# Kernel optimization log

Hardware: AMD Instinct MI355X
Metric: run time of the kernel (lower is better)

## Reference

```python
import jax, jax.numpy as jnp
import numpy as np

B, T, D = 4, 2048, 1024
H = 4                      # fla GatedLinearAttention default num_heads
K = D; V = D               # expand_k = expand_v = 1
DK = K // H; DV = V // H   # 256 each
LOW = 16                   # gate_low_rank_dim default
GLN = 16.0                 # gate_logit_normalizer default


def _layernorm(x, w, b, eps=1e-5):
    mu = x.mean(-1, keepdims=True)
    xc = x - mu
    var = (xc * xc).mean(-1, keepdims=True)
    return xc * jax.lax.rsqrt(var + eps) * w + b


def _rmsnorm(x, w, eps=1e-5):
    ms = (x * x).mean(-1, keepdims=True)
    return x * jax.lax.rsqrt(ms + eps) * w


def _gla_scan(q, k, v, gk):
    # q,k,gk: [B,T,H,DK]; v: [B,T,H,DV]
    scale = DK ** -0.5
    qT = jnp.moveaxis(q * scale, 1, 0)  # [T,B,H,DK]
    kT = jnp.moveaxis(k, 1, 0)
    vT = jnp.moveaxis(v, 1, 0)
    gT = jnp.moveaxis(gk, 1, 0)

    def step(h, inp):
        qt, kt, vt, gt = inp  # [B,H,DK]/[B,H,DV]
        h = h * jnp.exp(gt)[..., None] + kt[..., :, None] * vt[..., None, :]
        o = jnp.einsum('bhk,bhkv->bhv', qt, h)
        return h, o

    h0 = jnp.zeros((q.shape[0], H, DK, DV), q.dtype)
    _, oT = jax.lax.scan(step, h0, (qT, kT, vT, gT))
    return jnp.moveaxis(oT, 0, 1)  # [B,T,H,DV]


def setup_inputs() -> dict:
    key = jax.random.key(0)
    ks = jax.random.split(key, 12)
    rn = lambda k, s: jax.random.normal(k, s, jnp.float32) * 0.02
    return {
        'x': jax.random.normal(ks[0], (B, T, D), jnp.float32),
        'ln1_w': jnp.ones((D,), jnp.float32), 'ln1_b': jnp.zeros((D,), jnp.float32),
        'Wq': rn(ks[1], (D, K)), 'Wk': rn(ks[2], (D, K)), 'Wv': rn(ks[3], (D, V)),
        'Wg': rn(ks[4], (D, V)),
        'Wgk1': rn(ks[5], (D, LOW)), 'Wgk2': rn(ks[6], (LOW, K)), 'bgk2': jnp.zeros((K,), jnp.float32),
        'rms_w': jnp.ones((DV,), jnp.float32),
        'Wo': rn(ks[7], (V, D)),
        'ln2_w': jnp.ones((D,), jnp.float32), 'ln2_b': jnp.zeros((D,), jnp.float32),
        'W1': rn(ks[8], (D, 3 * D)), 'b1': jnp.zeros((3 * D,), jnp.float32),
        'W2': rn(ks[9], (3 * D, D)), 'b2': jnp.zeros((D,), jnp.float32),
    }


def reference(x, ln1_w, ln1_b, Wq, Wk, Wv, Wg, Wgk1, Wgk2, bgk2, rms_w, Wo,
              ln2_w, ln2_b, W1, b1, W2, b2):
    b, t = x.shape[0], x.shape[1]
    xn = _layernorm(x, ln1_w, ln1_b)
    q = (xn @ Wq).reshape(b, t, H, DK)
    k = (xn @ Wk).reshape(b, t, H, DK)
    v = (xn @ Wv).reshape(b, t, H, DV)
    # low-rank forget gate: logsigmoid / gate_logit_normalizer
    gk = (jax.nn.log_sigmoid((xn @ Wgk1) @ Wgk2 + bgk2) / GLN).reshape(b, t, H, DK)
    o = _gla_scan(q, k, v, gk)                      # [B,T,H,DV]
    g = (xn @ Wg).reshape(b, t, H, DV)              # output gate
    o = _rmsnorm(o, rms_w) * (g * jax.nn.sigmoid(g))  # gated RMSNorm (swish gate)
    o = o.reshape(b, t, V) @ Wo
    x = x + o
    xn2 = _layernorm(x, ln2_w, ln2_b)
    h = jax.nn.leaky_relu(xn2 @ W1 + b1, 0.01)
    h = h * h                                        # LeakyReLU^2
    x = x + (h @ W2 + b2)
    return x
```

## Files before the change

### kernel.cpp

```cpp
#include <hip/hip_runtime.h>
#include <math.h>

#define BB 4
#define TT 2048
#define DD 1024
#define HH 4
#define DK 256
#define DV 256
#define RR 8192
#define CHK 64
#define NCHK 32
#define SS ((size_t)RR * DD)

typedef __bf16 bf16x8 __attribute__((ext_vector_type(8)));
typedef float f32x4 __attribute__((ext_vector_type(4)));

static __device__ inline unsigned short f2bf(float f) {
  unsigned int u = __float_as_uint(f);
  unsigned int r = (u + 0x7fffu + ((u >> 16) & 1u)) >> 16;
  return (unsigned short)r;
}
static __device__ inline float bf2f(unsigned short h) {
  return __uint_as_float(((unsigned int)h) << 16);
}

static __device__ __forceinline__ void gload16(const unsigned short* g,
                                               unsigned short* l) {
  __builtin_amdgcn_global_load_lds(
      (const __attribute__((address_space(1))) void*)g,
      (__attribute__((address_space(3))) void*)l, 16, 0, 0);
}

__global__ __launch_bounds__(256) void ln_kernel(const float* __restrict__ x,
                                                 const float* __restrict__ w,
                                                 const float* __restrict__ b,
                                                 unsigned short* __restrict__ yb) {
  int row = blockIdx.x;
  const float* xr = x + (size_t)row * DD;
  unsigned short* ybr = yb + (size_t)row * DD;
  int tid = threadIdx.x;

  float4 v = ((const float4*)xr)[tid];
  float s = v.x + v.y + v.z + v.w;
  float ss = v.x * v.x + v.y * v.y + v.z * v.z + v.w * v.w;
#pragma unroll
  for (int o = 32; o > 0; o >>= 1) {
    s += __shfl_down(s, o);
    ss += __shfl_down(ss, o);
  }
  __shared__ float ls[4], lss[4];
  int wid = tid >> 6;
  if ((tid & 63) == 0) { ls[wid] = s; lss[wid] = ss; }
  __syncthreads();
  float sum = ls[0] + ls[1] + ls[2] + ls[3];
  float sumsq = lss[0] + lss[1] + lss[2] + lss[3];
  float mu = sum * (1.0f / DD);
  float var = sumsq * (1.0f / DD) - mu * mu;
  float rs = rsqrtf(var + 1e-5f);

  float4 wv = ((const float4*)w)[tid];
  float4 bv = ((const float4*)b)[tid];
  ushort4 ob;
  ob.x = f2bf((v.x - mu) * rs * wv.x + bv.x);
  ob.y = f2bf((v.y - mu) * rs * wv.y + bv.y);
  ob.z = f2bf((v.z - mu) * rs * wv.z + bv.z);
  ob.w = f2bf((v.w - mu) * rs * wv.w + bv.w);
  ((ushort4*)ybr)[tid] = ob;
}

__global__ __launch_bounds__(256) void transpose_cast(const float* __restrict__ W,
                                                      unsigned short* __restrict__ Wt,
                                                      int K, int N) {
  __shared__ float t[32][33];
  int k0 = blockIdx.y * 32, n0 = blockIdx.x * 32;
  int tid = threadIdx.x;
  int tx = tid & 31, ty = tid >> 5;
#pragma unroll
  for (int i = 0; i < 4; ++i)
    t[ty + i * 8][tx] = W[(size_t)(k0 + ty + i * 8) * N + n0 + tx];
  __syncthreads();
#pragma unroll
  for (int i = 0; i < 4; ++i)
    Wt[(size_t)(n0 + ty + i * 8) * K + k0 + tx] = f2bf(t[tx][ty + i * 8]);
}

template <int EPI, int OUTBF>
__global__ __launch_bounds__(256) void gemm_bf16(
    const unsigned short* __restrict__ A,
    const unsigned short* __restrict__ Bt,
    const float* __restrict__ bias, const float* __restrict__ Res,
    void* __restrict__ Cv, int M, int N, int K) {
  __shared__ unsigned short As[2][128 * 64];
  __shared__ unsigned short Bs[2][128 * 64];
  int tid = threadIdx.x;
  int nwg = gridDim.x * gridDim.y;
  int wg = blockIdx.y * gridDim.x + blockIdx.x;
  int cpx = nwg >> 3;
  wg = (wg & 7) * cpx + (wg >> 3);
  int m0 = (wg / gridDim.x) * 128, n0 = (wg % gridDim.x) * 128;
  int lane = tid & 63;
  int w64 = tid & 192;
  int wid = tid >> 6;
  int wm = (wid >> 1) * 64, wn = (wid & 1) * 64;
  int fr = lane & 15, fq = lane >> 4;

  f32x4 acc[4][4] = {};

  auto STAGE = [&](int buf, int k0) {
#pragma unroll
    for (int j = 0; j < 4; ++j) {
      int gl = j * 256 + tid;
      int row = gl >> 3;
      int gs = (gl & 7) ^ (row & 7);
      gload16(&A[(size_t)(m0 + row) * K + k0 + gs * 8],
              &As[buf][(size_t)(j * 256 + w64) * 8]);
      gload16(&Bt[(size_t)(n0 + row) * K + k0 + gs * 8],
              &Bs[buf][(size_t)(j * 256 + w64) * 8]);
    }
  };

  STAGE(0, 0);
  asm volatile("s_waitcnt vmcnt(0)");
  __syncthreads();

  int cur = 0;
  for (int k0 = 0; k0 < K; k0 += 64) {
    if (k0 + 64 < K) STAGE(cur ^ 1, k0 + 64);

#pragma unroll
    for (int ph = 0; ph < 2; ++ph) {
      bf16x8 af[4], bv[4];
#pragma unroll
      for (int i = 0; i < 4; ++i) {
        int ra = wm + i * 16 + fr;
        af[i] = *(const bf16x8*)&As[cur][ra * 64 + (((ph * 4 + fq) ^ (ra & 7)) * 8)];
        int rb = wn + i * 16 + fr;
        bv[i] = *(const bf16x8*)&Bs[cur][rb * 64 + (((ph * 4 + fq) ^ (rb & 7)) * 8)];
      }
#pragma unroll
      for (int i = 0; i < 4; ++i)
#pragma unroll
        for (int jj = 0; jj < 4; ++jj)
          acc[i][jj] = __builtin_amdgcn_mfma_f32_16x16x32_bf16(af[i], bv[jj],
                                                               acc[i][jj], 0, 0, 0);
    }
    __syncthreads();
    cur ^= 1;
  }

  int col = lane & 15;
  int rbase = (lane >> 4) * 4;
#pragma unroll
  for (int i = 0; i < 4; ++i) {
#pragma unroll
    for (int j = 0; j < 4; ++j) {
      int n = n0 + wn + j * 16 + col;
      float bvv = (EPI == 2 || EPI == 4) ? bias[n] : 0.0f;
#pragma unroll
      for (int r = 0; r < 4; ++r) {
        int m = m0 + wm + i * 16 + rbase + r;
        float vv = acc[i][j][r] + bvv;
        if (EPI == 2) {
          float t = vv > 0.0f ? vv : 0.01f * vv;
          vv = t * t;
        }
        if (EPI == 3 || EPI == 4) vv += Res[(size_t)m * N + n];
        if (EPI == 5) {
          ((unsigned short*)Cv)[(size_t)(n >> 10) * SS + (size_t)m * 1024 +
                                (n & 1023)] = f2bf(vv);
        } else if (OUTBF) {
          ((unsigned short*)Cv)[(size_t)m * N + n] = f2bf(vv);
        } else {
          ((float*)Cv)[(size_t)m * N + n] = vv;
        }
      }
    }
  }
}

__global__ __launch_bounds__(256) void gk_kernel(const unsigned short* __restrict__ xn,
                                                 const float* __restrict__ Wgk1,
                                                 const float* __restrict__ Wgk2,
                                                 const float* __restrict__ bgk2,
                                                 unsigned short* __restrict__ gk) {
  int row = blockIdx.x;
  const unsigned short* xr = xn + (size_t)row * DD;
  int tid = threadIdx.x;

  float t16[16];
#pragma unroll
  for (int j = 0; j < 16; ++j) t16[j] = 0.0f;

#pragma unroll
  for (int dd = 0; dd < 4; ++dd) {
    int d = tid + dd * 256;
    float xv = bf2f(xr[d]);
    const float4* wrow = (const float4*)(Wgk1 + (size_t)d * 16);
#pragma unroll
    for (int q = 0; q < 4; ++q) {
      float4 wq = wrow[q];
      t16[q * 4 + 0] += xv * wq.x;
      t16[q * 4 + 1] += xv * wq.y;
      t16[q * 4 + 2] += xv * wq.z;
      t16[q * 4 + 3] += xv * wq.w;
    }
  }
#pragma unroll
  for (int j = 0; j < 16; ++j) {
    float s = t16[j];
#pragma unroll
    for (int o = 32; o > 0; o >>= 1) s += __shfl_down(s, o);
    t16[j] = s;
  }
  __shared__ float tmp[4][16];
  __shared__ float tf[16];
  int wid = tid >> 6;
  if ((tid & 63) == 0) {
#pragma unroll
    for (int j = 0; j < 16; ++j) tmp[wid][j] = t16[j];
  }
  __syncthreads();
  if (tid < 16) tf[tid] = tmp[0][tid] + tmp[1][tid] + tmp[2][tid] + tmp[3][tid];
  __syncthreads();

  float tl[16];
#pragma unroll
  for (int j = 0; j < 16; ++j) tl[j] = tf[j];

#pragma unroll
  for (int jj = 0; jj < 4; ++jj) {
    int n = tid * 4 + jj;
    float z = bgk2[n];
#pragma unroll
    for (int j = 0; j < 16; ++j) z += tl[j] * Wgk2[j * 1024 + n];
    float ls = fminf(z, 0.0f) - log1pf(expf(-fabsf(z)));
    gk[(size_t)row * 1024 + n] = f2bf(ls * (1.0f / 16.0f));
  }
}

__global__ __launch_bounds__(256) void gate_chunk(const unsigned short* __restrict__ gk,
                                                  unsigned short* __restrict__ q,
                                                  unsigned short* __restrict__ k,
                                                  float* __restrict__ ebC) {
  int bid = blockIdx.x;
  int c = bid & 31;
  int h = (bid >> 5) & 3;
  int b = bid >> 7;
  int tid = threadIdx.x;
  size_t base = ((size_t)b * TT + c * CHK) * 1024 + h * 256 + tid;

  const float scale = 0.0625f;
  float cum = 0.0f;
  for (int t = 0; t < CHK; ++t) {
    size_t a = base + (size_t)t * 1024;
    cum += bf2f(gk[a]);
    q[a] = f2bf(bf2f(q[a]) * expf(cum) * scale);
    k[a] = f2bf(bf2f(k[a]) * expf(-cum));
  }
  ebC[((b * 4 + h) * NCHK + c) * 256 + tid] = expf(cum);
}

template <int WITHE>
__global__ __launch_bounds__(256) void trans_kernel(const unsigned short* __restrict__ in,
                                                    const float* __restrict__ ebC,
                                                    unsigned short* __restrict__ outT) {
  __shared__ unsigned short T[64][68];
  int bid = blockIdx.x;
  int dkt = bid & 3;
  int ct = (bid >> 2) & 31;
  int bh = bid >> 7;
  int b = bh >> 2, h = bh & 3;
  int tid = threadIdx.x;
  int r = tid >> 4;
  int c4 = (tid & 15) * 4;
  size_t srcbase = ((size_t)b * TT + ct * 64) * 1024 + h * 256 + dkt * 64;
#pragma unroll
  for (int i = 0; i < 4; ++i)
    *(ushort4*)&T[r + i * 16][c4] =
        *(const ushort4*)&in[srcbase + (size_t)(r + i * 16) * 1024 + c4];
  __syncthreads();
  size_t outbase = (size_t)bh * 524288 + (size_t)(dkt * 64) * 2048 + ct * 64;
  const float* ep = ebC + ((size_t)bh * 32 + ct) * 256 + dkt * 64;
#pragma unroll
  for (int i = 0; i < 4; ++i) {
    int dkl = r + i * 16;
    float e = WITHE ? ep[dkl] : 1.0f;
    ushort4 o;
    o.x = f2bf(bf2f(T[c4 + 0][dkl]) * e);
    o.y = f2bf(bf2f(T[c4 + 1][dkl]) * e);
    o.z = f2bf(bf2f(T[c4 + 2][dkl]) * e);
    o.w = f2bf(bf2f(T[c4 + 3][dkl]) * e);
    *(ushort4*)&outT[outbase + (size_t)dkl * 2048 + c4] = o;
  }
}

__global__ __launch_bounds__(256) void u_gemm(const unsigned short* __restrict__ khatT,
                                              const unsigned short* __restrict__ vT,
                                              unsigned short* __restrict__ UT) {
  __shared__ unsigned short As[128 * 64];
  __shared__ unsigned short Bs[128 * 64];
  int tid = threadIdx.x;
  int bid = blockIdx.x;
  int tile = bid & 3;
  int bhc = bid >> 2;
  int bh = bhc >> 5, c = bhc & 31;
  int m0 = (tile >> 1) * 128, n0 = (tile & 1) * 128;
  const unsigned short* Ab = vT + (size_t)bh * 524288 + c * 64;
  const unsigned short* Bb = khatT + (size_t)bh * 524288 + c * 64;
  unsigned short* Cb = UT + (size_t)bhc * 65536;

  int lane = tid & 63;
  int w64 = tid & 192;
  int wid = tid >> 6;
  int wm = (wid >> 1) * 64, wn = (wid & 1) * 64;
  int fr = lane & 15, fq = lane >> 4;

  f32x4 acc[4][4] = {};

#pragma unroll
  for (int j = 0; j < 4; ++j) {
    int gl = j * 256 + tid;
    int row = gl >> 3;
    int gs = (gl & 7) ^ (row & 7);
    gload16(&Ab[(size_t)(m0 + row) * 2048 + gs * 8],
            &As[(size_t)(j * 256 + w64) * 8]);
    gload16(&Bb[(size_t)(n0 + row) * 2048 + gs * 8],
            &Bs[(size_t)(j * 256 + w64) * 8]);
  }
  __syncthreads();

#pragma unroll
  for (int ph = 0; ph < 2; ++ph) {
    bf16x8 af[4], bv[4];
#pragma unroll
    for (int i = 0; i < 4; ++i) {
      int ra = wm + i * 16 + fr;
      af[i] = *(const bf16x8*)&As[ra * 64 + (((ph * 4 + fq) ^ (ra & 7)) * 8)];
      int rb = wn + i * 16 + fr;
      bv[i] = *(const bf16x8*)&Bs[rb * 64 + (((ph * 4 + fq) ^ (rb & 7)) * 8)];
    }
#pragma unroll
    for (int i = 0; i < 4; ++i)
#pragma unroll
      for (int jj = 0; jj < 4; ++jj)
        acc[i][jj] = __builtin_amdgcn_mfma_f32_16x16x32_bf16(af[i], bv[jj],
                                                             acc[i][jj], 0, 0, 0);
  }

  int col = lane & 15;
  int rbase = (lane >> 4) * 4;
#pragma unroll
  for (int i = 0; i < 4; ++i)
#pragma unroll
    for (int j = 0; j < 4; ++j) {
      int n = n0 + wn + j * 16 + col;
#pragma unroll
      for (int r = 0; r < 4; ++r) {
        int m = m0 + wm + i * 16 + rbase + r;
        Cb[(size_t)m * 256 + n] = f2bf(acc[i][j][r]);
      }
    }
}

__global__ __launch_bounds__(256) void hscan(unsigned short* __restrict__ UH,
                                             const float* __restrict__ ebC) {
  int bid = blockIdx.x;
  int bh = bid >> 8, dv = bid & 255;
  int tid = threadIdx.x;
  size_t base = ((size_t)bh * NCHK) * 65536 + (size_t)dv * 256 + tid;
  const float* ebb = ebC + (size_t)bh * NCHK * 256;
  float h = 0.0f;
  for (int c = 0; c < NCHK; ++c) {
    size_t a = base + (size_t)c * 65536;
    float u = bf2f(UH[a]);
    UH[a] = f2bf(h);
    h = ebb[c * 256 + tid] * h + u;
  }
}

__global__ __launch_bounds__(256) void attn_fused(
    const unsigned short* __restrict__ qt, const unsigned short* __restrict__ kt,
    const unsigned short* __restrict__ vT, const unsigned short* __restrict__ HT,
    const unsigned short* __restrict__ gp, const float* __restrict__ rw,
    unsigned short* __restrict__ og) {
  __shared__ unsigned short Qs[64 * 264];
  __shared__ unsigned short KVH[256 * 72];
  __shared__ unsigned short Sb[64 * 64];
  __shared__ float red[64][4];

  int bid = blockIdx.x;
  int c = bid & 31;
  int bh = bid >> 5;
  int b = bh >> 2, h = bh & 3;
  size_t rowbase = ((size_t)b * TT + c * 64) * 1024 + h * 256;
  size_t vtbase = (size_t)bh * 524288 + c * 64;
  size_t htbase = ((size_t)(bh * 32 + c)) * 65536;
  int tid = threadIdx.x;
  int lane = tid & 63;
  int w = tid >> 6;
  int fr = lane & 15, fq = lane >> 4;

#pragma unroll
  for (int i = 0; i < 8; ++i) {
    int gg = tid + i * 256;
    int row = gg >> 5, gc = gg & 31;
    *(bf16x8*)&Qs[row * 264 + gc * 8] =
        *(const bf16x8*)&qt[rowbase + (size_t)row * 1024 + gc * 8];
    *(bf16x8*)&KVH[row * 264 + gc * 8] =
        *(const bf16x8*)&kt[rowbase + (size_t)row * 1024 + gc * 8];
  }
  __syncthreads();

  {
    f32x4 accs[4] = {};
#pragma unroll
    for (int ks = 0; ks < 8; ++ks) {
      bf16x8 af = *(const bf16x8*)&Qs[(w * 16 + fr) * 264 + ks * 32 + fq * 8];
#pragma unroll
      for (int si = 0; si < 4; ++si) {
        bf16x8 bf_ = *(const bf16x8*)&KVH[(si * 16 + fr) * 264 + ks * 32 + fq * 8];
        accs[si] = __builtin_amdgcn_mfma_f32_16x16x32_bf16(af, bf_, accs[si], 0, 0, 0);
      }
    }
#pragma unroll
    for (int si = 0; si < 4; ++si) {
#pragma unroll
      for (int r = 0; r < 4; ++r) {
        int t = w * 16 + fq * 4 + r;
        int s = si * 16 + fr;
        float val = (s <= t) ? accs[si][r] : 0.0f;
        Sb[t * 64 + (((s >> 3) ^ (t & 7)) * 8) + (s & 7)] = f2bf(val);
      }
    }
  }
  __syncthreads();

#pragma unroll
  for (int i = 0; i < 8; ++i) {
    int gg = tid + i * 256;
    int dv = gg >> 3, gc = gg & 7;
    *(bf16x8*)&KVH[dv * 72 + gc * 8] =
        *(const bf16x8*)&vT[vtbase + (size_t)dv * 2048 + gc * 8];
  }
  __syncthreads();

  int dv0 = w * 64;
  f32x4 acc[4][4] = {};

#pragma unroll
  for (int ks = 0; ks < 2; ++ks) {
    bf16x8 af[4], bv[4];
#pragma unroll
    for (int ti = 0; ti < 4; ++ti) {
      int t = ti * 16 + fr;
      af[ti] = *(const bf16x8*)&Sb[t * 64 + (((ks * 4 + fq) ^ (t & 7)) * 8)];
    }
#pragma unroll
    for (int nj = 0; nj < 4; ++nj)
      bv[nj] = *(const bf16x8*)&KVH[(dv0 + nj * 16 + fr) * 72 + ks * 32 + fq * 8];
#pragma unroll
    for (int ti = 0; ti < 4; ++ti)
#pragma unroll
      for (int nj = 0; nj < 4; ++nj)
        acc[ti][nj] = __builtin_amdgcn_mfma_f32_16x16x32_bf16(af[ti], bv[nj],
                                                              acc[ti][nj], 0, 0, 0);
  }

  for (int k4 = 0; k4 < 4; ++k4) {
    __syncthreads();
#pragma unroll
    for (int i = 0; i < 8; ++i) {
      int gg = tid + i * 256;
      int dv = gg >> 3, gc = gg & 7;
      *(bf16x8*)&KVH[dv * 72 + gc * 8] =
          *(const bf16x8*)&HT[htbase + (size_t)dv * 256 + k4 * 64 + gc * 8];
    }
    __syncthreads();
#pragma unroll
    for (int ks = 0; ks < 2; ++ks) {
      bf16x8 af[4], bv[4];
#pragma unroll
      for (int ti = 0; ti < 4; ++ti)
        af[ti] = *(const bf16x8*)&Qs[(ti * 16 + fr) * 264 + k4 * 64 + ks * 32 + fq * 8];
#pragma unroll
      for (int nj = 0; nj < 4; ++nj)
        bv[nj] = *(const bf16x8*)&KVH[(dv0 + nj * 16 + fr) * 72 + ks * 32 + fq * 8];
#pragma unroll
      for (int ti = 0; ti < 4; ++ti)
#pragma unroll
        for (int nj = 0; nj < 4; ++nj)
          acc[ti][nj] = __builtin_amdgcn_mfma_f32_16x16x32_bf16(af[ti], bv[nj],
                                                                acc[ti][nj], 0, 0, 0);
    }
  }

  float rstd[4][4];
#pragma unroll
  for (int ti = 0; ti < 4; ++ti) {
#pragma unroll
    for (int r = 0; r < 4; ++r) {
      float s = 0.0f;
#pragma unroll
      for (int nj = 0; nj < 4; ++nj) {
        float v = acc[ti][nj][r];
        s += v * v;
      }
      s += __shfl_xor(s, 1);
      s += __shfl_xor(s, 2);
      s += __shfl_xor(s, 4);
      s += __shfl_xor(s, 8);
      rstd[ti][r] = s;
    }
  }
  if (fr == 0) {
#pragma unroll
    for (int ti = 0; ti < 4; ++ti)
#pragma unroll
      for (int r = 0; r < 4; ++r)
        red[ti * 16 + fq * 4 + r][w] = rstd[ti][r];
  }
  __syncthreads();
#pragma unroll
  for (int ti = 0; ti < 4; ++ti) {
#pragma unroll
    for (int r = 0; r < 4; ++r) {
      int t = ti * 16 + fq * 4 + r;
      float tot = red[t][0] + red[t][1] + red[t][2] + red[t][3];
      rstd[ti][r] = rsqrtf(tot * (1.0f / 256.0f) + 1e-5f);
    }
  }
#pragma unroll
  for (int ti = 0; ti < 4; ++ti) {
#pragma unroll
    for (int nj = 0; nj < 4; ++nj) {
      int dv = dv0 + nj * 16 + fr;
      float rwv = rw[dv];
#pragma unroll
      for (int r = 0; r < 4; ++r) {
        int t = ti * 16 + fq * 4 + r;
        float gv = bf2f(gp[rowbase + (size_t)t * 1024 + dv]);
        float sw = gv / (1.0f + expf(-gv));
        og[rowbase + (size_t)t * 1024 + dv] =
            f2bf(acc[ti][nj][r] * rstd[ti][r] * rwv * sw);
      }
    }
  }
}

extern "C" void kernel_launch(void* const* d_in, const int* in_sizes, int n_in,
                              void* d_out, int out_size, void* d_ws,
                              size_t ws_size, hipStream_t stream) {
  const float* x = (const float*)d_in[0];
  const float* ln1_w = (const float*)d_in[1];
  const float* ln1_b = (const float*)d_in[2];
  const float* Wq = (const float*)d_in[3];
  const float* Wk = (const float*)d_in[4];
  const float* Wv = (const float*)d_in[5];
  const float* Wg = (const float*)d_in[6];
  const float* Wgk1 = (const float*)d_in[7];
  const float* Wgk2 = (const float*)d_in[8];
  const float* bgk2 = (const float*)d_in[9];
  const float* rms_w = (const float*)d_in[10];
  const float* Wo = (const float*)d_in[11];
  const float* ln2_w = (const float*)d_in[12];
  const float* ln2_b = (const float*)d_in[13];
  const float* W1 = (const float*)d_in[14];
  const float* b1 = (const float*)d_in[15];
  const float* W2 = (const float*)d_in[16];
  const float* b2 = (const float*)d_in[17];
  float* out = (float*)d_out;

  const size_t S = SS;
  unsigned short* actb = (unsigned short*)d_ws;
  unsigned short* qb = actb + S;
  unsigned short* kb = qb + S;
  unsigned short* vb = kb + S;
  unsigned short* gb = vb + S;
  unsigned short* gkb = gb + S;
  unsigned short* ogb = gkb + S;
  unsigned short* UH = ogb + 2 * S;
  float* ebC = (float*)(UH + 4 * S);
  unsigned short* Wqkvgt = (unsigned short*)(ebC + 131072);
  unsigned short* Wot = Wqkvgt + 4194304;
  unsigned short* W1t = Wot + 1048576;
  unsigned short* W2t = W1t + 3145728;
  unsigned short* khatT = gkb;
  unsigned short* vT = actb;
  float* x1 = (float*)kb;
  unsigned short* hb = UH;

  dim3 blk(256);

  transpose_cast<<<dim3(32, 32), blk, 0, stream>>>(Wq, Wqkvgt, 1024, 1024);
  transpose_cast<<<dim3(32, 32), blk, 0, stream>>>(Wk, Wqkvgt + 1048576, 1024, 1024);
  transpose_cast<<<dim3(32, 32), blk, 0, stream>>>(Wv, Wqkvgt + 2097152, 1024, 1024);
  transpose_cast<<<dim3(32, 32), blk, 0, stream>>>(Wg, Wqkvgt + 3145728, 1024, 1024);
  transpose_cast<<<dim3(32, 32), blk, 0, stream>>>(Wo, Wot, 1024, 1024);
  transpose_cast<<<dim3(96, 32), blk, 0, stream>>>(W1, W1t, 1024, 3072);
  transpose_cast<<<dim3(32, 96), blk, 0, stream>>>(W2, W2t, 3072, 1024);

  ln_kernel<<<RR, blk, 0, stream>>>(x, ln1_w, ln1_b, actb);

  dim3 g4096(4096 / 128, RR / 128);
  gemm_bf16<5, 1><<<g4096, blk, 0, stream>>>(actb, Wqkvgt, nullptr, nullptr, qb,
                                             RR, 4096, 1024);

  gk_kernel<<<RR, blk, 0, stream>>>(actb, Wgk1, Wgk2, bgk2, gkb);

  gate_chunk<<<BB * HH * NCHK, blk, 0, stream>>>(gkb, qb, kb, ebC);

  trans_kernel<1><<<16 * 32 * 4, blk, 0, stream>>>(kb, ebC, khatT);
  trans_kernel<0><<<16 * 32 * 4, blk, 0, stream>>>(vb, ebC, vT);

  u_gemm<<<16 * NCHK * 4, blk, 0, stream>>>(khatT, vT, UH);
  hscan<<<16 * 256, blk, 0, stream>>>(UH, ebC);

  attn_fused<<<16 * NCHK, blk, 0, stream>>>(qb, kb, vT, UH, gb, rms_w, ogb);

  dim3 g1024(1024 / 128, RR / 128);
  gemm_bf16<3, 0><<<g1024, blk, 0, stream>>>(ogb, Wot, nullptr, x, x1, RR, 1024, 1024);

  ln_kernel<<<RR, blk, 0, stream>>>(x1, ln2_w, ln2_b, actb);

  dim3 g3072(3072 / 128, RR / 128);
  gemm_bf16<2, 1><<<g3072, blk, 0, stream>>>(actb, W1t, b1, nullptr, hb, RR, 3072, 1024);

  gemm_bf16<4, 0><<<g1024, blk, 0, stream>>>(hb, W2t, b2, x1, out, RR, 1024, 3072);
}
```

Baseline: 445.2 us.

## Batch gk kernel over 16 rows, merge weight transposes, prefetch scan loads

The low-rank gate kernel now handles 16 rows per block. It stages the rows and a bf16 copy of Wgk1 in shared memory and keeps Wgk2 in registers, so the weights are reused across rows and there are fewer launches. Wgk1 is rounded to bf16, which slightly changes the gate numerics. The five square weight transposes become a single launch using a z-indexed grid. gate_chunk and hscan now load all their serial inputs into registers before running the recurrence, which shortens the memory-latency chain but uses more registers.

```diff
diff --git a/kernel.cpp b/kernel.cpp
--- a/kernel.cpp
+++ b/kernel.cpp
@@ -82,6 +82,27 @@
 #pragma unroll
   for (int i = 0; i < 4; ++i)
     Wt[(size_t)(n0 + ty + i * 8) * K + k0 + tx] = f2bf(t[tx][ty + i * 8]);
+}
+
+struct P5 {
+  const float* w[5];
+  unsigned short* o[5];
+};
+__global__ __launch_bounds__(256) void transpose5(P5 p) {
+  __shared__ float t[32][33];
+  int z = blockIdx.z;
+  const float* W = p.w[z];
+  unsigned short* Wt = p.o[z];
+  int k0 = blockIdx.y * 32, n0 = blockIdx.x * 32;
+  int tid = threadIdx.x;
+  int tx = tid & 31, ty = tid >> 5;
+#pragma unroll
+  for (int i = 0; i < 4; ++i)
+    t[ty + i * 8][tx] = W[(size_t)(k0 + ty + i * 8) * 1024 + n0 + tx];
+  __syncthreads();
+#pragma unroll
+  for (int i = 0; i < 4; ++i)
+    Wt[(size_t)(n0 + ty + i * 8) * 1024 + k0 + tx] = f2bf(t[tx][ty + i * 8]);
 }
 
 template <int EPI, int OUTBF>
@@ -183,58 +204,90 @@
                                                  const float* __restrict__ Wgk2,
                                                  const float* __restrict__ bgk2,
                                                  unsigned short* __restrict__ gk) {
-  int row = blockIdx.x;
-  const unsigned short* xr = xn + (size_t)row * DD;
-  int tid = threadIdx.x;
-
-  float t16[16];
-#pragma unroll
-  for (int j = 0; j < 16; ++j) t16[j] = 0.0f;
-
-#pragma unroll
-  for (int dd = 0; dd < 4; ++dd) {
-    int d = tid + dd * 256;
-    float xv = bf2f(xr[d]);
-    const float4* wrow = (const float4*)(Wgk1 + (size_t)d * 16);
-#pragma unroll
-    for (int q = 0; q < 4; ++q) {
-      float4 wq = wrow[q];
-      t16[q * 4 + 0] += xv * wq.x;
-      t16[q * 4 + 1] += xv * wq.y;
-      t16[q * 4 + 2] += xv * wq.z;
-      t16[q * 4 + 3] += xv * wq.w;
-    }
-  }
-#pragma unroll
-  for (int j = 0; j < 16; ++j) {
-    float s = t16[j];
-#pragma unroll
-    for (int o = 32; o > 0; o >>= 1) s += __shfl_down(s, o);
-    t16[j] = s;
-  }
-  __shared__ float tmp[4][16];
-  __shared__ float tf[16];
-  int wid = tid >> 6;
-  if ((tid & 63) == 0) {
-#pragma unroll
-    for (int j = 0; j < 16; ++j) tmp[wid][j] = t16[j];
-  }
-  __syncthreads();
-  if (tid < 16) tf[tid] = tmp[0][tid] + tmp[1][tid] + tmp[2][tid] + tmp[3][tid];
-  __syncthreads();
-
-  float tl[16];
-#pragma unroll
-  for (int j = 0; j < 16; ++j) tl[j] = tf[j];
-
-#pragma unroll
-  for (int jj = 0; jj < 4; ++jj) {
-    int n = tid * 4 + jj;
-    float z = bgk2[n];
-#pragma unroll
-    for (int j = 0; j < 16; ++j) z += tl[j] * Wgk2[j * 1024 + n];
-    float ls = fminf(z, 0.0f) - log1pf(expf(-fabsf(z)));
-    gk[(size_t)row * 1024 + n] = f2bf(ls * (1.0f / 16.0f));
+  __shared__ unsigned short Xs[16 * 1024];
+  __shared__ unsigned short W1s[1024 * 16];
+  __shared__ float Ts[16][16];
+  int r0 = blockIdx.x * 16;
+  int tid = threadIdx.x;
+
+#pragma unroll
+  for (int i = 0; i < 16; ++i) {
+    int idx = tid + i * 256;
+    ((ushort4*)Xs)[idx] = ((const ushort4*)(xn + (size_t)r0 * 1024))[idx];
+  }
+#pragma unroll
+  for (int i = 0; i < 16; ++i) {
+    int idx = tid + i * 256;
+    float4 w = ((const float4*)Wgk1)[idx];
+    ushort4 hh;
+    hh.x = f2bf(w.x); hh.y = f2bf(w.y); hh.z = f2bf(w.z); hh.w = f2bf(w.w);
+    ((ushort4*)W1s)[idx] = hh;
+  }
+  __syncthreads();
+
+  {
+    int r = tid >> 4, part = tid & 15;
+    float t16[16];
+#pragma unroll
+    for (int j = 0; j < 16; ++j) t16[j] = 0.0f;
+    for (int dd = 0; dd < 64; ++dd) {
+      int d = dd * 16 + part;
+      float xv = bf2f(Xs[r * 1024 + d]);
+      const ushort4* wr = (const ushort4*)&W1s[d * 16];
+#pragma unroll
+      for (int q4 = 0; q4 < 4; ++q4) {
+        ushort4 w = wr[q4];
+        t16[q4 * 4 + 0] += xv * bf2f(w.x);
+        t16[q4 * 4 + 1] += xv * bf2f(w.y);
+        t16[q4 * 4 + 2] += xv * bf2f(w.z);
+        t16[q4 * 4 + 3] += xv * bf2f(w.w);
+      }
+    }
+#pragma unroll
+    for (int j = 0; j < 16; ++j) {
+      float s = t16[j];
+      s += __shfl_xor(s, 1);
+      s += __shfl_xor(s, 2);
+      s += __shfl_xor(s, 4);
+      s += __shfl_xor(s, 8);
+      t16[j] = s;
+    }
+    if (part == 0) {
+#pragma unroll
+      for (int j = 0; j < 16; ++j) Ts[r][j] = t16[j];
+    }
+  }
+  __syncthreads();
+
+  {
+    float w2[16][4];
+#pragma unroll
+    for (int j = 0; j < 16; ++j) {
+      float4 wv = *(const float4*)&Wgk2[(size_t)j * 1024 + tid * 4];
+      w2[j][0] = wv.x; w2[j][1] = wv.y; w2[j][2] = wv.z; w2[j][3] = wv.w;
+    }
+    float4 bv = *(const float4*)&bgk2[tid * 4];
+    float bb[4] = {bv.x, bv.y, bv.z, bv.w};
+#pragma unroll
+    for (int r = 0; r < 16; ++r) {
+      ushort4 outv;
+      unsigned short* op = (unsigned short*)&outv;
+#pragma unroll
+      for (int jj = 0; jj < 4; ++jj) {
+        float z = bb[jj];
+#pragma unroll
+        for (int j = 0; j < 16; ++j) z += Ts[r][j] * w2[j][jj];
+        float lsg = fminf(z, 0.0f) - log1pf(expf(-fabsf(z)));
+        op[jj] = f2bf(lsg * (1.0f / 16.0f));
+      }
+      *(ushort4*)&Xs[r * 1024 + tid * 4] = outv;
+    }
+  }
+  __syncthreads();
+#pragma unroll
+  for (int i = 0; i < 16; ++i) {
+    int idx = tid + i * 256;
+    ((ushort4*)(gk + (size_t)r0 * 1024))[idx] = ((const ushort4*)Xs)[idx];
   }
 }
 
@@ -249,15 +302,24 @@
   int tid = threadIdx.x;
   size_t base = ((size_t)b * TT + c * CHK) * 1024 + h * 256 + tid;
 
+  float cums[64];
+#pragma unroll
+  for (int t = 0; t < 64; ++t) cums[t] = bf2f(gk[base + (size_t)t * 1024]);
+  float cum = 0.0f;
+#pragma unroll
+  for (int t = 0; t < 64; ++t) {
+    cum += cums[t];
+    cums[t] = cum;
+  }
+  ebC[((b * 4 + h) * NCHK + c) * 256 + tid] = expf(cum);
+
   const float scale = 0.0625f;
-  float cum = 0.0f;
-  for (int t = 0; t < CHK; ++t) {
+#pragma unroll
+  for (int t = 0; t < 64; ++t) {
     size_t a = base + (size_t)t * 1024;
-    cum += bf2f(gk[a]);
-    q[a] = f2bf(bf2f(q[a]) * expf(cum) * scale);
-    k[a] = f2bf(bf2f(k[a]) * expf(-cum));
-  }
-  ebC[((b * 4 + h) * NCHK + c) * 256 + tid] = expf(cum);
+    q[a] = f2bf(bf2f(q[a]) * expf(cums[t]) * scale);
+    k[a] = f2bf(bf2f(k[a]) * expf(-cums[t]));
+  }
 }
 
 template <int WITHE>
@@ -368,13 +430,18 @@
   int bh = bid >> 8, dv = bid & 255;
   int tid = threadIdx.x;
   size_t base = ((size_t)bh * NCHK) * 65536 + (size_t)dv * 256 + tid;
-  const float* ebb = ebC + (size_t)bh * NCHK * 256;
+  const float* ebb = ebC + (size_t)bh * NCHK * 256 + tid;
+
+  float u[32], e[32];
+#pragma unroll
+  for (int c = 0; c < 32; ++c) u[c] = bf2f(UH[base + (size_t)c * 65536]);
+#pragma unroll
+  for (int c = 0; c < 32; ++c) e[c] = ebb[c * 256];
   float h = 0.0f;
-  for (int c = 0; c < NCHK; ++c) {
-    size_t a = base + (size_t)c * 65536;
-    float u = bf2f(UH[a]);
-    UH[a] = f2bf(h);
-    h = ebb[c * 256 + tid] * h + u;
+#pragma unroll
+  for (int c = 0; c < 32; ++c) {
+    UH[base + (size_t)c * 65536] = f2bf(h);
+    h = e[c] * h + u[c];
   }
 }
 
@@ -591,11 +658,13 @@
 
   dim3 blk(256);
 
-  transpose_cast<<<dim3(32, 32), blk, 0, stream>>>(Wq, Wqkvgt, 1024, 1024);
-  transpose_cast<<<dim3(32, 32), blk, 0, stream>>>(Wk, Wqkvgt + 1048576, 1024, 1024);
-  transpose_cast<<<dim3(32, 32), blk, 0, stream>>>(Wv, Wqkvgt + 2097152, 1024, 1024);
-  transpose_cast<<<dim3(32, 32), blk, 0, stream>>>(Wg, Wqkvgt + 3145728, 1024, 1024);
-  transpose_cast<<<dim3(32, 32), blk, 0, stream>>>(Wo, Wot, 1024, 1024);
+  P5 p5;
+  p5.w[0] = Wq;  p5.o[0] = Wqkvgt;
+  p5.w[1] = Wk;  p5.o[1] = Wqkvgt + 1048576;
+  p5.w[2] = Wv;  p5.o[2] = Wqkvgt + 2097152;
+  p5.w[3] = Wg;  p5.o[3] = Wqkvgt + 3145728;
+  p5.w[4] = Wo;  p5.o[4] = Wot;
+  transpose5<<<dim3(32, 32, 5), blk, 0, stream>>>(p5);
   transpose_cast<<<dim3(96, 32), blk, 0, stream>>>(W1, W1t, 1024, 3072);
   transpose_cast<<<dim3(32, 96), blk, 0, stream>>>(W2, W2t, 3072, 1024);
 
@@ -605,7 +674,7 @@
   gemm_bf16<5, 1><<<g4096, blk, 0, stream>>>(actb, Wqkvgt, nullptr, nullptr, qb,
                                              RR, 4096, 1024);
 
-  gk_kernel<<<RR, blk, 0, stream>>>(actb, Wgk1, Wgk2, bgk2, gkb);
+  gk_kernel<<<RR / 16, blk, 0, stream>>>(actb, Wgk1, Wgk2, bgk2, gkb);
 
   gate_chunk<<<BB * HH * NCHK, blk, 0, stream>>>(gkb, qb, kb, ebC);
 
```

After: 426.1 us. 4.3% less time.
